# Performance work log

Hardware: AMD Instinct MI355X
Metric: run time of the kernel (lower is better)

The kernel has to match this reference:

```python
import jax, jax.numpy as jnp
import numpy as np

NUM_ATOMS = 262144
INPUT_DIM = 256
HIDDEN_DIM = 256
NUM_HEADS = 8
HEAD_DIM = HIDDEN_DIM // NUM_HEADS
NUM_GRAPHS = 2048
SCALE = float(np.sqrt(HEAD_DIM))


def setup_inputs() -> dict:
    key = jax.random.key(0)
    ks = jax.random.split(key, 9)
    x = jax.random.normal(ks[0], (NUM_ATOMS, INPUT_DIM), dtype=jnp.float32)
    batch = jnp.sort(jax.random.randint(ks[1], (NUM_ATOMS,), 0, NUM_GRAPHS, dtype=jnp.int32))
    queries = jax.random.normal(ks[2], (NUM_HEADS, HEAD_DIM), dtype=jnp.float32)
    s_in = 1.0 / np.sqrt(INPUT_DIM)
    s_h = 1.0 / np.sqrt(HIDDEN_DIM)
    Wk = jax.random.uniform(ks[3], (INPUT_DIM, HIDDEN_DIM), jnp.float32, -s_in, s_in)
    bk = jax.random.uniform(ks[4], (HIDDEN_DIM,), jnp.float32, -s_in, s_in)
    Wv = jax.random.uniform(ks[5], (INPUT_DIM, HIDDEN_DIM), jnp.float32, -s_in, s_in)
    bv = jax.random.uniform(ks[6], (HIDDEN_DIM,), jnp.float32, -s_in, s_in)
    Wo = jax.random.uniform(ks[7], (HIDDEN_DIM, INPUT_DIM), jnp.float32, -s_h, s_h)
    bo = jax.random.uniform(ks[8], (INPUT_DIM,), jnp.float32, -s_h, s_h)
    return {"x": x, "batch": batch, "queries": queries, "Wk": Wk, "bk": bk,
            "Wv": Wv, "bv": bv, "Wo": Wo, "bo": bo}


def reference(x, batch, queries, Wk, bk, Wv, bv, Wo, bo):
    N = x.shape[0]
    # projections: [N, hidden] -> [N, H, D]
    keys = (x @ Wk + bk).reshape(N, NUM_HEADS, HEAD_DIM)
    values = (x @ Wv + bv).reshape(N, NUM_HEADS, HEAD_DIM)
    # per-node, per-head attention logits against learned queries
    scores = jnp.einsum('nhd,hd->nh', keys, queries) / SCALE  # [N, H]
    # segment-wise (per-graph) stable softmax over nodes
    seg_max = jax.ops.segment_max(scores, batch, num_segments=NUM_GRAPHS)  # [B, H]
    w = jnp.exp(scores - seg_max[batch])                                   # [N, H]
    denom = jax.ops.segment_sum(w, batch, num_segments=NUM_GRAPHS)         # [B, H]
    w = w / denom[batch]
    # weighted sum of values per graph: [B, H, D]
    attended = jax.ops.segment_sum(w[:, :, None] * values, batch, num_segments=NUM_GRAPHS)
    attended = attended.reshape(NUM_GRAPHS, HIDDEN_DIM)
    return attended @ Wo + bo  # [B, input_dim]
```

## Files before the change

### kernel.cpp

```cpp
#include <hip/hip_runtime.h>

#define N_ATOMS 262144
#define NGRAPH  2048
#define INV_SCALE 0.17677669529663687f

typedef float f32x2 __attribute__((ext_vector_type(2)));
typedef float f32x4 __attribute__((ext_vector_type(4)));

__device__ __forceinline__ f32x2 pk_mul(f32x2 a, f32x2 b) {
  f32x2 d; asm("v_pk_mul_f32 %0, %1, %2" : "=v"(d) : "v"(a), "v"(b)); return d;
}
__device__ __forceinline__ f32x2 pk_fma(f32x2 a, f32x2 b, f32x2 c) {
  f32x2 d; asm("v_pk_fma_f32 %0, %1, %2, %3" : "=v"(d) : "v"(a), "v"(b), "v"(c)); return d;
}
__device__ __forceinline__ f32x2 pk_fma_blo(f32x2 a, f32x2 b, f32x2 c) {
  f32x2 d; asm("v_pk_fma_f32 %0, %1, %2, %3 op_sel_hi:[0,1,1]"
               : "=v"(d) : "v"(a), "v"(b), "v"(c)); return d;
}
__device__ __forceinline__ f32x2 pk_fma_bhi(f32x2 a, f32x2 b, f32x2 c) {
  f32x2 d; asm("v_pk_fma_f32 %0, %1, %2, %3 op_sel:[1,0,0]"
               : "=v"(d) : "v"(a), "v"(b), "v"(c)); return d;
}
__device__ __forceinline__ f32x4 ldnt4(const float* p) {
  return __builtin_nontemporal_load(reinterpret_cast<const f32x4*>(p));
}

__global__ void k_pre(const float* __restrict__ Wk, const float* __restrict__ bk,
                      const float* __restrict__ q, const int* __restrict__ batch,
                      float* __restrict__ P, float* __restrict__ c,
                      int* __restrict__ bounds) {
  if (blockIdx.x < 8) {
    int h = blockIdx.x, i = threadIdx.x;
    float s = 0.f;
    #pragma unroll
    for (int d = 0; d < 32; ++d)
      s = fmaf(Wk[i * 256 + h * 32 + d], q[h * 32 + d], s);
    P[h * 256 + i] = s;
    if (i == 0) {
      float cc = 0.f;
      #pragma unroll
      for (int d = 0; d < 32; ++d) cc = fmaf(bk[h * 32 + d], q[h * 32 + d], cc);
      c[h] = cc;
    }
  } else {
    int g = (blockIdx.x - 8) * 256 + threadIdx.x;
    if (g >= NGRAPH) return;
    int lo = 0, hi = N_ATOMS;
    while (lo < hi) {
      int mid = (lo + hi) >> 1;
      if (batch[mid] < g) lo = mid + 1; else hi = mid;
    }
    bounds[2 * g] = lo;
    if (g > 0) bounds[2 * g - 1] = lo;
    if (g == NGRAPH - 1) bounds[2 * g + 1] = N_ATOMS;
  }
}

__device__ __forceinline__ float fold8(float acc[8], int lane) {
  {
    int m = lane & 8;
    float nw[4];
    #pragma unroll
    for (int j = 0; j < 4; ++j) {
      float snd = m ? acc[j] : acc[j + 4];
      float rcv = __shfl_xor(snd, 8, 64);
      nw[j] = (m ? acc[j + 4] : acc[j]) + rcv;
    }
    #pragma unroll
    for (int j = 0; j < 4; ++j) acc[j] = nw[j];
  }
  {
    int m = lane & 16;
    float nw[2];
    #pragma unroll
    for (int j = 0; j < 2; ++j) {
      float snd = m ? acc[j] : acc[j + 2];
      float rcv = __shfl_xor(snd, 16, 64);
      nw[j] = (m ? acc[j + 2] : acc[j]) + rcv;
    }
    acc[0] = nw[0]; acc[1] = nw[1];
  }
  float r;
  {
    int m = lane & 32;
    float snd = m ? acc[0] : acc[1];
    float rcv = __shfl_xor(snd, 32, 64);
    r = (m ? acc[1] : acc[0]) + rcv;
  }
  r += __shfl_xor(r, 1, 64);
  r += __shfl_xor(r, 2, 64);
  r += __shfl_xor(r, 4, 64);
  return r;
}

__global__ __launch_bounds__(256, 4) void k_fused(const float* __restrict__ x,
                                                  const float* __restrict__ P,
                                                  const float* __restrict__ c,
                                                  const int* __restrict__ bounds,
                                                  float* __restrict__ Ag) {
  int b = blockIdx.x;
  int s = bounds[2 * b], e = bounds[2 * b + 1];
  int t = threadIdx.x, lane = t & 63, wv = t >> 6;
  int h = ((lane >> 1) & 4) | ((lane >> 3) & 2) | ((lane >> 5) & 1);

  f32x2 Pl2[8][2];
  #pragma unroll
  for (int k = 0; k < 8; ++k) {
    f32x4 pv = *reinterpret_cast<const f32x4*>(P + k * 256 + 4 * lane);
    Pl2[k][0] = __builtin_shufflevector(pv, pv, 0, 1);
    Pl2[k][1] = __builtin_shufflevector(pv, pv, 2, 3);
  }
  float cl = c[h];

  f32x2 A2[8][2];
  #pragma unroll
  for (int k = 0; k < 8; ++k) { A2[k][0] = (f32x2)0.f; A2[k][1] = (f32x2)0.f; }
  float dacc = 0.f;

  __shared__ float elds[4][2][8];
  __shared__ float Asc[4][2][256];
  __shared__ float dws[4][8];
  __shared__ float dinvs[8];

  for (int n0 = s + 2 * wv; n0 < e; n0 += 8) {
    bool has2 = (n0 + 1) < e;
    int n1 = has2 ? n0 + 1 : n0;
    f32x4 xq0 = ldnt4(x + (size_t)n0 * 256 + 4 * lane);
    f32x4 xq1 = ldnt4(x + (size_t)n1 * 256 + 4 * lane);
    f32x2 x0lo = __builtin_shufflevector(xq0, xq0, 0, 1);
    f32x2 x0hi = __builtin_shufflevector(xq0, xq0, 2, 3);
    f32x2 x1lo = __builtin_shufflevector(xq1, xq1, 0, 1);
    f32x2 x1hi = __builtin_shufflevector(xq1, xq1, 2, 3);

    float acc0[8], acc1[8];
    #pragma unroll
    for (int k = 0; k < 8; ++k) {
      f32x2 p0 = pk_fma(x0hi, Pl2[k][1], pk_mul(x0lo, Pl2[k][0]));
      f32x2 p1 = pk_fma(x1hi, Pl2[k][1], pk_mul(x1lo, Pl2[k][0]));
      acc0[k] = p0[0] + p0[1];
      acc1[k] = p1[0] + p1[1];
    }
    float r0 = fold8(acc0, lane);
    float r1 = fold8(acc1, lane);
    float ev0 = __expf((r0 + cl) * INV_SCALE);
    float ev1 = __expf((r1 + cl) * INV_SCALE);
    ev1 = has2 ? ev1 : 0.f;
    dacc += ev0 + ev1;

    if ((lane & 7) == 0) {
      elds[wv][0][h] = ev0;
      elds[wv][1][h] = ev1;
    }
    f32x4 ea03 = *reinterpret_cast<const f32x4*>(&elds[wv][0][0]);
    f32x4 ea47 = *reinterpret_cast<const f32x4*>(&elds[wv][0][4]);
    f32x4 eb03 = *reinterpret_cast<const f32x4*>(&elds[wv][1][0]);
    f32x4 eb47 = *reinterpret_cast<const f32x4*>(&elds[wv][1][4]);
    f32x2 ea[4] = { __builtin_shufflevector(ea03, ea03, 0, 1),
                    __builtin_shufflevector(ea03, ea03, 2, 3),
                    __builtin_shufflevector(ea47, ea47, 0, 1),
                    __builtin_shufflevector(ea47, ea47, 2, 3) };
    f32x2 eb[4] = { __builtin_shufflevector(eb03, eb03, 0, 1),
                    __builtin_shufflevector(eb03, eb03, 2, 3),
                    __builtin_shufflevector(eb47, eb47, 0, 1),
                    __builtin_shufflevector(eb47, eb47, 2, 3) };
    #pragma unroll
    for (int j = 0; j < 4; ++j) {
      A2[2*j][0]   = pk_fma_blo(ea[j], x0lo, A2[2*j][0]);
      A2[2*j][1]   = pk_fma_blo(ea[j], x0hi, A2[2*j][1]);
      A2[2*j+1][0] = pk_fma_bhi(ea[j], x0lo, A2[2*j+1][0]);
      A2[2*j+1][1] = pk_fma_bhi(ea[j], x0hi, A2[2*j+1][1]);
      A2[2*j][0]   = pk_fma_blo(eb[j], x1lo, A2[2*j][0]);
      A2[2*j][1]   = pk_fma_blo(eb[j], x1hi, A2[2*j][1]);
      A2[2*j+1][0] = pk_fma_bhi(eb[j], x1lo, A2[2*j+1][0]);
      A2[2*j+1][1] = pk_fma_bhi(eb[j], x1hi, A2[2*j+1][1]);
    }
  }

  if ((lane & 7) == 0) dws[wv][h] = dacc;
  __syncthreads();
  if (t < 8) {
    float ds = dws[0][t] + dws[1][t] + dws[2][t] + dws[3][t];
    dinvs[t] = ds > 0.f ? 1.0f / ds : 0.f;
  }
  #pragma unroll
  for (int p = 0; p < 4; ++p) {
    float4 a0, a1;
    a0.x = A2[2*p][0][0];   a0.y = A2[2*p][0][1];
    a0.z = A2[2*p][1][0];   a0.w = A2[2*p][1][1];
    a1.x = A2[2*p+1][0][0]; a1.y = A2[2*p+1][0][1];
    a1.z = A2[2*p+1][1][0]; a1.w = A2[2*p+1][1][1];
    *reinterpret_cast<float4*>(&Asc[wv][0][4 * lane]) = a0;
    *reinterpret_cast<float4*>(&Asc[wv][1][4 * lane]) = a1;
    __syncthreads();
    float v0 = Asc[0][0][t] + Asc[1][0][t] + Asc[2][0][t] + Asc[3][0][t];
    float v1 = Asc[0][1][t] + Asc[1][1][t] + Asc[2][1][t] + Asc[3][1][t];
    Ag[(size_t)b * 2048 + (2*p) * 256 + t]   = v0 * dinvs[2*p];
    Ag[(size_t)b * 2048 + (2*p+1) * 256 + t] = v1 * dinvs[2*p+1];
    __syncthreads();
  }
}

__global__ __launch_bounds__(256) void k_out(const float* __restrict__ Ag,
                                             const int* __restrict__ bounds,
                                             const float* __restrict__ Wv,
                                             const float* __restrict__ bv,
                                             const float* __restrict__ Wo,
                                             const float* __restrict__ bo,
                                             float* __restrict__ out) {
  __shared__ float Alds[4 * 2048];
  __shared__ float attlds[4 * 256];
  __shared__ float eflag[4];
  int b0 = blockIdx.x * 4;
  int t = threadIdx.x;
  #pragma unroll
  for (int r = 0; r < 32; ++r) {
    int idx = r * 256 + t;
    Alds[idx] = Ag[(size_t)b0 * 2048 + idx];
  }
  if (t < 4) {
    int s = bounds[2 * (b0 + t)], e = bounds[2 * (b0 + t) + 1];
    eflag[t] = (e > s) ? 1.0f : 0.0f;
  }
  __syncthreads();
  int h = t >> 5;
  float bvk = bv[t];
  float acc[4];
  #pragma unroll
  for (int g = 0; g < 4; ++g) acc[g] = 0.f;
  for (int i4 = 0; i4 < 64; ++i4) {
    float aa[4][4];
    #pragma unroll
    for (int g = 0; g < 4; ++g) {
      float4 v = *reinterpret_cast<const float4*>(&Alds[g * 2048 + h * 256 + i4 * 4]);
      aa[g][0] = v.x; aa[g][1] = v.y; aa[g][2] = v.z; aa[g][3] = v.w;
    }
    #pragma unroll
    for (int j = 0; j < 4; ++j) {
      float wvv = Wv[(size_t)(i4 * 4 + j) * 256 + t];
      #pragma unroll
      for (int g = 0; g < 4; ++g) acc[g] = fmaf(aa[g][j], wvv, acc[g]);
    }
  }
  #pragma unroll
  for (int g = 0; g < 4; ++g) attlds[g * 256 + t] = acc[g] + bvk * eflag[g];
  __syncthreads();
  float boj = bo[t];
  float o[4];
  #pragma unroll
  for (int g = 0; g < 4; ++g) o[g] = boj;
  for (int k4 = 0; k4 < 64; ++k4) {
    float aa[4][4];
    #pragma unroll
    for (int g = 0; g < 4; ++g) {
      float4 v = *reinterpret_cast<const float4*>(&attlds[g * 256 + k4 * 4]);
      aa[g][0] = v.x; aa[g][1] = v.y; aa[g][2] = v.z; aa[g][3] = v.w;
    }
    #pragma unroll
    for (int j = 0; j < 4; ++j) {
      float wo = Wo[(size_t)(k4 * 4 + j) * 256 + t];
      #pragma unroll
      for (int g = 0; g < 4; ++g) o[g] = fmaf(aa[g][j], wo, o[g]);
    }
  }
  #pragma unroll
  for (int g = 0; g < 4; ++g) out[(size_t)(b0 + g) * 256 + t] = o[g];
}

extern "C" void kernel_launch(void* const* d_in, const int* in_sizes, int n_in,
                              void* d_out, int out_size, void* d_ws, size_t ws_size,
                              hipStream_t stream) {
  const float* x   = (const float*)d_in[0];
  const int*   bat = (const int*)d_in[1];
  const float* q   = (const float*)d_in[2];
  const float* Wk  = (const float*)d_in[3];
  const float* bk  = (const float*)d_in[4];
  const float* Wv  = (const float*)d_in[5];
  const float* bv  = (const float*)d_in[6];
  const float* Wo  = (const float*)d_in[7];
  const float* bo  = (const float*)d_in[8];
  float* out = (float*)d_out;

  float* ws = (float*)d_ws;
  float* P      = ws;
  float* c      = ws + 2048;
  int*   bounds = (int*)(ws + 4096);
  float* Ag     = ws + 8192;

  k_pre<<<16, 256, 0, stream>>>(Wk, bk, q, bat, P, c, bounds);
  k_fused<<<NGRAPH, 256, 0, stream>>>(x, P, c, bounds, Ag);
  k_out<<<NGRAPH / 4, 256, 0, stream>>>(Ag, bounds, Wv, bv, Wo, bo, out);
}
```

Baseline: 97.47 us.

## Process four atoms per wave iteration and stream P rows from cache

Each wave now loads four atom rows per iteration instead of two, and batches the cross-lane shuffle reductions for all four. This gives more memory-level parallelism and better amortizes the shuffle latency. To offset the larger live state, the per-lane P projection is no longer held in registers and is reloaded from global/L1 inside the loop. That adds repeated loads in exchange for fewer registers.

```diff
diff --git a/kernel.cpp b/kernel.cpp
--- a/kernel.cpp
+++ b/kernel.cpp
@@ -56,41 +56,45 @@
   }
 }
 
-__device__ __forceinline__ float fold8(float acc[8], int lane) {
-  {
-    int m = lane & 8;
+__device__ __forceinline__ void fold8_x4(float acc[4][8], int lane, float r[4]) {
+  int m8 = lane & 8;
+  #pragma unroll
+  for (int a = 0; a < 4; ++a) {
     float nw[4];
     #pragma unroll
     for (int j = 0; j < 4; ++j) {
-      float snd = m ? acc[j] : acc[j + 4];
+      float snd = m8 ? acc[a][j] : acc[a][j + 4];
       float rcv = __shfl_xor(snd, 8, 64);
-      nw[j] = (m ? acc[j + 4] : acc[j]) + rcv;
-    }
-    #pragma unroll
-    for (int j = 0; j < 4; ++j) acc[j] = nw[j];
-  }
-  {
-    int m = lane & 16;
+      nw[j] = (m8 ? acc[a][j + 4] : acc[a][j]) + rcv;
+    }
+    #pragma unroll
+    for (int j = 0; j < 4; ++j) acc[a][j] = nw[j];
+  }
+  int m16 = lane & 16;
+  #pragma unroll
+  for (int a = 0; a < 4; ++a) {
     float nw[2];
     #pragma unroll
     for (int j = 0; j < 2; ++j) {
-      float snd = m ? acc[j] : acc[j + 2];
+      float snd = m16 ? acc[a][j] : acc[a][j + 2];
       float rcv = __shfl_xor(snd, 16, 64);
-      nw[j] = (m ? acc[j + 2] : acc[j]) + rcv;
-    }
-    acc[0] = nw[0]; acc[1] = nw[1];
-  }
-  float r;
-  {
-    int m = lane & 32;
-    float snd = m ? acc[0] : acc[1];
+      nw[j] = (m16 ? acc[a][j + 2] : acc[a][j]) + rcv;
+    }
+    acc[a][0] = nw[0]; acc[a][1] = nw[1];
+  }
+  int m32 = lane & 32;
+  #pragma unroll
+  for (int a = 0; a < 4; ++a) {
+    float snd = m32 ? acc[a][0] : acc[a][1];
     float rcv = __shfl_xor(snd, 32, 64);
-    r = (m ? acc[1] : acc[0]) + rcv;
-  }
-  r += __shfl_xor(r, 1, 64);
-  r += __shfl_xor(r, 2, 64);
-  r += __shfl_xor(r, 4, 64);
-  return r;
+    r[a] = (m32 ? acc[a][1] : acc[a][0]) + rcv;
+  }
+  #pragma unroll
+  for (int a = 0; a < 4; ++a) r[a] += __shfl_xor(r[a], 1, 64);
+  #pragma unroll
+  for (int a = 0; a < 4; ++a) r[a] += __shfl_xor(r[a], 2, 64);
+  #pragma unroll
+  for (int a = 0; a < 4; ++a) r[a] += __shfl_xor(r[a], 4, 64);
 }
 
 __global__ __launch_bounds__(256, 4) void k_fused(const float* __restrict__ x,
@@ -103,76 +107,70 @@
   int t = threadIdx.x, lane = t & 63, wv = t >> 6;
   int h = ((lane >> 1) & 4) | ((lane >> 3) & 2) | ((lane >> 5) & 1);
 
-  f32x2 Pl2[8][2];
-  #pragma unroll
-  for (int k = 0; k < 8; ++k) {
-    f32x4 pv = *reinterpret_cast<const f32x4*>(P + k * 256 + 4 * lane);
-    Pl2[k][0] = __builtin_shufflevector(pv, pv, 0, 1);
-    Pl2[k][1] = __builtin_shufflevector(pv, pv, 2, 3);
-  }
   float cl = c[h];
+  const float* Prow = P + 4 * lane;
 
   f32x2 A2[8][2];
   #pragma unroll
   for (int k = 0; k < 8; ++k) { A2[k][0] = (f32x2)0.f; A2[k][1] = (f32x2)0.f; }
   float dacc = 0.f;
 
-  __shared__ float elds[4][2][8];
+  __shared__ float elds[4][4][8];
   __shared__ float Asc[4][2][256];
   __shared__ float dws[4][8];
   __shared__ float dinvs[8];
 
-  for (int n0 = s + 2 * wv; n0 < e; n0 += 8) {
-    bool has2 = (n0 + 1) < e;
-    int n1 = has2 ? n0 + 1 : n0;
-    f32x4 xq0 = ldnt4(x + (size_t)n0 * 256 + 4 * lane);
-    f32x4 xq1 = ldnt4(x + (size_t)n1 * 256 + 4 * lane);
-    f32x2 x0lo = __builtin_shufflevector(xq0, xq0, 0, 1);
-    f32x2 x0hi = __builtin_shufflevector(xq0, xq0, 2, 3);
-    f32x2 x1lo = __builtin_shufflevector(xq1, xq1, 0, 1);
-    f32x2 x1hi = __builtin_shufflevector(xq1, xq1, 2, 3);
-
-    float acc0[8], acc1[8];
+  for (int n0 = s + 4 * wv; n0 < e; n0 += 16) {
+    f32x4 xq[4];
+    #pragma unroll
+    for (int a = 0; a < 4; ++a) {
+      int na = n0 + a; na = na < e ? na : e - 1;
+      xq[a] = ldnt4(x + (size_t)na * 256 + 4 * lane);
+    }
+    float acc[4][8];
     #pragma unroll
     for (int k = 0; k < 8; ++k) {
-      f32x2 p0 = pk_fma(x0hi, Pl2[k][1], pk_mul(x0lo, Pl2[k][0]));
-      f32x2 p1 = pk_fma(x1hi, Pl2[k][1], pk_mul(x1lo, Pl2[k][0]));
-      acc0[k] = p0[0] + p0[1];
-      acc1[k] = p1[0] + p1[1];
-    }
-    float r0 = fold8(acc0, lane);
-    float r1 = fold8(acc1, lane);
-    float ev0 = __expf((r0 + cl) * INV_SCALE);
-    float ev1 = __expf((r1 + cl) * INV_SCALE);
-    ev1 = has2 ? ev1 : 0.f;
-    dacc += ev0 + ev1;
-
+      f32x4 pv = *reinterpret_cast<const f32x4*>(Prow + k * 256);
+      f32x2 plo = __builtin_shufflevector(pv, pv, 0, 1);
+      f32x2 phi = __builtin_shufflevector(pv, pv, 2, 3);
+      #pragma unroll
+      for (int a = 0; a < 4; ++a) {
+        f32x2 xlo = __builtin_shufflevector(xq[a], xq[a], 0, 1);
+        f32x2 xhi = __builtin_shufflevector(xq[a], xq[a], 2, 3);
+        f32x2 p = pk_fma(xhi, phi, pk_mul(xlo, plo));
+        acc[a][k] = p[0] + p[1];
+      }
+    }
+    float r[4];
+    fold8_x4(acc, lane, r);
+    float ev[4];
+    #pragma unroll
+    for (int a = 0; a < 4; ++a) {
+      float ee = __expf((r[a] + cl) * INV_SCALE);
+      ev[a] = ((n0 + a) < e) ? ee : 0.f;
+      dacc += ev[a];
+    }
     if ((lane & 7) == 0) {
-      elds[wv][0][h] = ev0;
-      elds[wv][1][h] = ev1;
-    }
-    f32x4 ea03 = *reinterpret_cast<const f32x4*>(&elds[wv][0][0]);
-    f32x4 ea47 = *reinterpret_cast<const f32x4*>(&elds[wv][0][4]);
-    f32x4 eb03 = *reinterpret_cast<const f32x4*>(&elds[wv][1][0]);
-    f32x4 eb47 = *reinterpret_cast<const f32x4*>(&elds[wv][1][4]);
-    f32x2 ea[4] = { __builtin_shufflevector(ea03, ea03, 0, 1),
-                    __builtin_shufflevector(ea03, ea03, 2, 3),
-                    __builtin_shufflevector(ea47, ea47, 0, 1),
-                    __builtin_shufflevector(ea47, ea47, 2, 3) };
-    f32x2 eb[4] = { __builtin_shufflevector(eb03, eb03, 0, 1),
-                    __builtin_shufflevector(eb03, eb03, 2, 3),
-                    __builtin_shufflevector(eb47, eb47, 0, 1),
-                    __builtin_shufflevector(eb47, eb47, 2, 3) };
-    #pragma unroll
-    for (int j = 0; j < 4; ++j) {
-      A2[2*j][0]   = pk_fma_blo(ea[j], x0lo, A2[2*j][0]);
-      A2[2*j][1]   = pk_fma_blo(ea[j], x0hi, A2[2*j][1]);
-      A2[2*j+1][0] = pk_fma_bhi(ea[j], x0lo, A2[2*j+1][0]);
-      A2[2*j+1][1] = pk_fma_bhi(ea[j], x0hi, A2[2*j+1][1]);
-      A2[2*j][0]   = pk_fma_blo(eb[j], x1lo, A2[2*j][0]);
-      A2[2*j][1]   = pk_fma_blo(eb[j], x1hi, A2[2*j][1]);
-      A2[2*j+1][0] = pk_fma_bhi(eb[j], x1lo, A2[2*j+1][0]);
-      A2[2*j+1][1] = pk_fma_bhi(eb[j], x1hi, A2[2*j+1][1]);
+      #pragma unroll
+      for (int a = 0; a < 4; ++a) elds[wv][a][h] = ev[a];
+    }
+    #pragma unroll
+    for (int a = 0; a < 4; ++a) {
+      f32x4 eA = *reinterpret_cast<const f32x4*>(&elds[wv][a][0]);
+      f32x4 eB = *reinterpret_cast<const f32x4*>(&elds[wv][a][4]);
+      f32x2 ep[4] = { __builtin_shufflevector(eA, eA, 0, 1),
+                      __builtin_shufflevector(eA, eA, 2, 3),
+                      __builtin_shufflevector(eB, eB, 0, 1),
+                      __builtin_shufflevector(eB, eB, 2, 3) };
+      f32x2 xlo = __builtin_shufflevector(xq[a], xq[a], 0, 1);
+      f32x2 xhi = __builtin_shufflevector(xq[a], xq[a], 2, 3);
+      #pragma unroll
+      for (int j = 0; j < 4; ++j) {
+        A2[2*j][0]   = pk_fma_blo(ep[j], xlo, A2[2*j][0]);
+        A2[2*j][1]   = pk_fma_blo(ep[j], xhi, A2[2*j][1]);
+        A2[2*j+1][0] = pk_fma_bhi(ep[j], xlo, A2[2*j+1][0]);
+        A2[2*j+1][1] = pk_fma_bhi(ep[j], xhi, A2[2*j+1][1]);
+      }
     }
   }
 
```

After: 136.7 us. 1.4x slower.

## Double-buffer x rows through LDS with async global_load_lds prefetch

Applied to the files above, without the earlier changes.

Replaces direct nontemporal global loads of x rows with asynchronous global_load_lds copies into a per-wave double-buffered LDS area. The next pair of rows is prefetched while the current pair is processed, using vmcnt waits to synchronize. The goal is to hide global memory latency in the per-graph streaming loop, at the cost of extra LDS traffic and capacity (16 KB), which may reduce occupancy. Tail handling clamps prefetch indices to e-1, so the last iteration issues redundant loads.

```diff
diff --git a/kernel.cpp b/kernel.cpp
--- a/kernel.cpp
+++ b/kernel.cpp
@@ -21,8 +21,11 @@
   f32x2 d; asm("v_pk_fma_f32 %0, %1, %2, %3 op_sel:[1,0,0]"
                : "=v"(d) : "v"(a), "v"(b), "v"(c)); return d;
 }
-__device__ __forceinline__ f32x4 ldnt4(const float* p) {
-  return __builtin_nontemporal_load(reinterpret_cast<const f32x4*>(p));
+
+__device__ __forceinline__ void stage_row(const float* gsrc, float* lds_dst) {
+  __builtin_amdgcn_global_load_lds(
+      (const __attribute__((address_space(1))) unsigned int*)gsrc,
+      (__attribute__((address_space(3))) unsigned int*)lds_dst, 16, 0, 0);
 }
 
 __global__ void k_pre(const float* __restrict__ Wk, const float* __restrict__ bk,
@@ -117,16 +120,34 @@
   for (int k = 0; k < 8; ++k) { A2[k][0] = (f32x2)0.f; A2[k][1] = (f32x2)0.f; }
   float dacc = 0.f;
 
+  __shared__ float xs[4][2][2][256];
   __shared__ float elds[4][2][8];
   __shared__ float Asc[4][2][256];
   __shared__ float dws[4][8];
   __shared__ float dinvs[8];
 
-  for (int n0 = s + 2 * wv; n0 < e; n0 += 8) {
+  const float* xl = x + 4 * lane;
+  int n_first = s + 2 * wv;
+
+  if (n_first < e) {
+    int r1 = (n_first + 1 < e) ? n_first + 1 : e - 1;
+    stage_row(xl + (size_t)n_first * 256, &xs[wv][0][0][0]);
+    stage_row(xl + (size_t)r1 * 256, &xs[wv][0][1][0]);
+  }
+
+  int cur = 0;
+  for (int n0 = n_first; n0 < e; n0 += 8) {
+    int nn = n0 + 8;
+    int p0 = (nn < e) ? nn : e - 1;
+    int p1 = (nn + 1 < e) ? nn + 1 : e - 1;
+    stage_row(xl + (size_t)p0 * 256, &xs[wv][cur ^ 1][0][0]);
+    stage_row(xl + (size_t)p1 * 256, &xs[wv][cur ^ 1][1][0]);
+    asm volatile("s_waitcnt vmcnt(2)" ::: "memory");
+    __builtin_amdgcn_sched_barrier(0);
+
+    f32x4 xq0 = *reinterpret_cast<const f32x4*>(&xs[wv][cur][0][4 * lane]);
+    f32x4 xq1 = *reinterpret_cast<const f32x4*>(&xs[wv][cur][1][4 * lane]);
     bool has2 = (n0 + 1) < e;
-    int n1 = has2 ? n0 + 1 : n0;
-    f32x4 xq0 = ldnt4(x + (size_t)n0 * 256 + 4 * lane);
-    f32x4 xq1 = ldnt4(x + (size_t)n1 * 256 + 4 * lane);
     f32x2 x0lo = __builtin_shufflevector(xq0, xq0, 0, 1);
     f32x2 x0hi = __builtin_shufflevector(xq0, xq0, 2, 3);
     f32x2 x1lo = __builtin_shufflevector(xq1, xq1, 0, 1);
@@ -135,10 +156,10 @@
     float acc0[8], acc1[8];
     #pragma unroll
     for (int k = 0; k < 8; ++k) {
-      f32x2 p0 = pk_fma(x0hi, Pl2[k][1], pk_mul(x0lo, Pl2[k][0]));
-      f32x2 p1 = pk_fma(x1hi, Pl2[k][1], pk_mul(x1lo, Pl2[k][0]));
-      acc0[k] = p0[0] + p0[1];
-      acc1[k] = p1[0] + p1[1];
+      f32x2 p0v = pk_fma(x0hi, Pl2[k][1], pk_mul(x0lo, Pl2[k][0]));
+      f32x2 p1v = pk_fma(x1hi, Pl2[k][1], pk_mul(x1lo, Pl2[k][0]));
+      acc0[k] = p0v[0] + p0v[1];
+      acc1[k] = p1v[0] + p1v[1];
     }
     float r0 = fold8(acc0, lane);
     float r1 = fold8(acc1, lane);
@@ -174,7 +195,9 @@
       A2[2*j+1][0] = pk_fma_bhi(eb[j], x1lo, A2[2*j+1][0]);
       A2[2*j+1][1] = pk_fma_bhi(eb[j], x1hi, A2[2*j+1][1]);
     }
-  }
+    cur ^= 1;
+  }
+  asm volatile("s_waitcnt vmcnt(0)" ::: "memory");
 
   if ((lane & 7) == 0) dws[wv][h] = dacc;
   __syncthreads();
```

New measurement: 104.7 us. +7.5%, slower.

## Software-pipeline atom loop with rotating register prefetch of x rows

Applied to the files above, without the earlier changes.

Restructures the per-wave atom loop so each wave handles one atom per step, interleaved with stride 4, using three rotating registers that prefetch x rows several atoms ahead. The value accumulation for one atom is deferred behind the next load and dot product, so global-load latency overlaps with compute. Out-of-range indices are clamped to the last atom and their weights zeroed. This adds extra redundant clamped loads at segment tails and more live registers.

```diff
diff --git a/kernel.cpp b/kernel.cpp
--- a/kernel.cpp
+++ b/kernel.cpp
@@ -117,62 +117,69 @@
   for (int k = 0; k < 8; ++k) { A2[k][0] = (f32x2)0.f; A2[k][1] = (f32x2)0.f; }
   float dacc = 0.f;
 
-  __shared__ float elds[4][2][8];
+  __shared__ float elds[4][3][8];
   __shared__ float Asc[4][2][256];
   __shared__ float dws[4][8];
   __shared__ float dinvs[8];
 
-  for (int n0 = s + 2 * wv; n0 < e; n0 += 8) {
-    bool has2 = (n0 + 1) < e;
-    int n1 = has2 ? n0 + 1 : n0;
-    f32x4 xq0 = ldnt4(x + (size_t)n0 * 256 + 4 * lane);
-    f32x4 xq1 = ldnt4(x + (size_t)n1 * 256 + 4 * lane);
-    f32x2 x0lo = __builtin_shufflevector(xq0, xq0, 0, 1);
-    f32x2 x0hi = __builtin_shufflevector(xq0, xq0, 2, 3);
-    f32x2 x1lo = __builtin_shufflevector(xq1, xq1, 0, 1);
-    f32x2 x1hi = __builtin_shufflevector(xq1, xq1, 2, 3);
-
-    float acc0[8], acc1[8];
+  const float* xl = x + 4 * lane;
+
+  auto ca = [&](int a) { return a < e ? a : (e - 1); };
+
+  auto acc_step = [&](f32x4 XQ, int ES) {
+    f32x4 eA = *reinterpret_cast<const f32x4*>(&elds[wv][ES][0]);
+    f32x4 eB = *reinterpret_cast<const f32x4*>(&elds[wv][ES][4]);
+    f32x2 ep[4] = { __builtin_shufflevector(eA, eA, 0, 1),
+                    __builtin_shufflevector(eA, eA, 2, 3),
+                    __builtin_shufflevector(eB, eB, 0, 1),
+                    __builtin_shufflevector(eB, eB, 2, 3) };
+    f32x2 xlo = __builtin_shufflevector(XQ, XQ, 0, 1);
+    f32x2 xhi = __builtin_shufflevector(XQ, XQ, 2, 3);
+    #pragma unroll
+    for (int j = 0; j < 4; ++j) {
+      A2[2*j][0]   = pk_fma_blo(ep[j], xlo, A2[2*j][0]);
+      A2[2*j][1]   = pk_fma_blo(ep[j], xhi, A2[2*j][1]);
+      A2[2*j+1][0] = pk_fma_bhi(ep[j], xlo, A2[2*j+1][0]);
+      A2[2*j+1][1] = pk_fma_bhi(ep[j], xhi, A2[2*j+1][1]);
+    }
+  };
+
+  auto dot_step = [&](f32x4 XQ, int ES, int aidx) {
+    f32x2 xlo = __builtin_shufflevector(XQ, XQ, 0, 1);
+    f32x2 xhi = __builtin_shufflevector(XQ, XQ, 2, 3);
+    float acc[8];
     #pragma unroll
     for (int k = 0; k < 8; ++k) {
-      f32x2 p0 = pk_fma(x0hi, Pl2[k][1], pk_mul(x0lo, Pl2[k][0]));
-      f32x2 p1 = pk_fma(x1hi, Pl2[k][1], pk_mul(x1lo, Pl2[k][0]));
-      acc0[k] = p0[0] + p0[1];
-      acc1[k] = p1[0] + p1[1];
-    }
-    float r0 = fold8(acc0, lane);
-    float r1 = fold8(acc1, lane);
-    float ev0 = __expf((r0 + cl) * INV_SCALE);
-    float ev1 = __expf((r1 + cl) * INV_SCALE);
-    ev1 = has2 ? ev1 : 0.f;
-    dacc += ev0 + ev1;
-
-    if ((lane & 7) == 0) {
-      elds[wv][0][h] = ev0;
-      elds[wv][1][h] = ev1;
-    }
-    f32x4 ea03 = *reinterpret_cast<const f32x4*>(&elds[wv][0][0]);
-    f32x4 ea47 = *reinterpret_cast<const f32x4*>(&elds[wv][0][4]);
-    f32x4 eb03 = *reinterpret_cast<const f32x4*>(&elds[wv][1][0]);
-    f32x4 eb47 = *reinterpret_cast<const f32x4*>(&elds[wv][1][4]);
-    f32x2 ea[4] = { __builtin_shufflevector(ea03, ea03, 0, 1),
-                    __builtin_shufflevector(ea03, ea03, 2, 3),
-                    __builtin_shufflevector(ea47, ea47, 0, 1),
-                    __builtin_shufflevector(ea47, ea47, 2, 3) };
-    f32x2 eb[4] = { __builtin_shufflevector(eb03, eb03, 0, 1),
-                    __builtin_shufflevector(eb03, eb03, 2, 3),
-                    __builtin_shufflevector(eb47, eb47, 0, 1),
-                    __builtin_shufflevector(eb47, eb47, 2, 3) };
-    #pragma unroll
-    for (int j = 0; j < 4; ++j) {
-      A2[2*j][0]   = pk_fma_blo(ea[j], x0lo, A2[2*j][0]);
-      A2[2*j][1]   = pk_fma_blo(ea[j], x0hi, A2[2*j][1]);
-      A2[2*j+1][0] = pk_fma_bhi(ea[j], x0lo, A2[2*j+1][0]);
-      A2[2*j+1][1] = pk_fma_bhi(ea[j], x0hi, A2[2*j+1][1]);
-      A2[2*j][0]   = pk_fma_blo(eb[j], x1lo, A2[2*j][0]);
-      A2[2*j][1]   = pk_fma_blo(eb[j], x1hi, A2[2*j][1]);
-      A2[2*j+1][0] = pk_fma_bhi(eb[j], x1lo, A2[2*j+1][0]);
-      A2[2*j+1][1] = pk_fma_bhi(eb[j], x1hi, A2[2*j+1][1]);
+      f32x2 p = pk_fma(xhi, Pl2[k][1], pk_mul(xlo, Pl2[k][0]));
+      acc[k] = p[0] + p[1];
+    }
+    float r = fold8(acc, lane);
+    float ev = __expf((r + cl) * INV_SCALE);
+    ev = (aidx < e) ? ev : 0.f;
+    dacc += ev;
+    if ((lane & 7) == 0) elds[wv][ES][h] = ev;
+  };
+
+  int i0 = s + wv;
+  if (i0 < e) {
+    int G = (e - i0 + 3) >> 2;
+    int M = (G + 3) / 3;
+    f32x4 xqA = ldnt4(xl + (size_t)ca(i0) * 256);
+    f32x4 xqB = ldnt4(xl + (size_t)ca(i0 + 4) * 256);
+    f32x4 xqC = {0.f, 0.f, 0.f, 0.f};
+    if ((lane & 7) == 0) elds[wv][2][h] = 0.f;
+    int a = i0;
+    for (int m = 0; m < M; ++m) {
+      acc_step(xqC, 2);
+      xqC = ldnt4(xl + (size_t)ca(a + 8) * 256);
+      dot_step(xqA, 0, a);
+      acc_step(xqA, 0);
+      xqA = ldnt4(xl + (size_t)ca(a + 12) * 256);
+      dot_step(xqB, 1, a + 4);
+      acc_step(xqB, 1);
+      xqB = ldnt4(xl + (size_t)ca(a + 16) * 256);
+      dot_step(xqC, 2, a + 8);
+      a += 12;
     }
   }
 
```

After: 101.8 us. 1.04x slower.
